# Performance work log

Hardware: AMD Instinct MI355X
Metric: run time of the kernel (lower is better)

## Reference

```python
import jax, jax.numpy as jnp
import numpy as np

# dims
B, S, D, H, DH, M, L, V, BS, NR = 4, 2048, 512, 8, 64, 2048, 6, 32000, 64, 3
NB = S // BS  # 32 blocks


def _block_plan(nb, seed):
    """BigBird block connectivity: 2 global + 3 window + NR random blocks per query block.
    Returns idx [nb, K] int32 and validity mask [nb, K] bool (dedup + edge handling)."""
    rng = np.random.RandomState(seed)
    K = 5 + NR
    idx = np.zeros((nb, K), np.int32)
    msk = np.zeros((nb, K), bool)
    for i in range(nb):
        fixed = {0, nb - 1} | {j for j in (i - 1, i, i + 1) if 0 <= j < nb}
        rest = [j for j in range(nb) if j not in fixed]
        rnd = rng.choice(rest, size=min(NR, len(rest)), replace=False) if rest else []
        sel = sorted(fixed | set(int(r) for r in rnd))
        idx[i, :len(sel)] = sel
        msk[i, :len(sel)] = True
    return jnp.asarray(idx), jnp.asarray(msk)


def _posemb():
    pos = np.arange(S, dtype=np.float32)[:, None]
    div = np.exp(np.arange(0, D, 2, dtype=np.float32) * (-np.log(10000.0) / D))
    pe = np.zeros((S, D), np.float32)
    pe[:, 0::2] = np.sin(pos * div)
    pe[:, 1::2] = np.cos(pos * div)
    return jnp.asarray(pe)


def _ln(x, scale, bias):
    m = jnp.mean(x, axis=-1, keepdims=True)
    v = jnp.mean(jnp.square(x - m), axis=-1, keepdims=True)
    return (x - m) * jax.lax.rsqrt(v + 1e-6) * scale + bias


def _bigbird_attn(x, key_mask, wq, wk, wv, wo, idx, bmask):
    # x: [B,S,D]; idx/bmask: [NB,K]
    q = jnp.einsum('bsd,dhe->bshe', x, wq).reshape(B, NB, BS, H, DH)
    k = jnp.einsum('bsd,dhe->bshe', x, wk).reshape(B, NB, BS, H, DH)
    v = jnp.einsum('bsd,dhe->bshe', x, wv).reshape(B, NB, BS, H, DH)
    kg = k[:, idx]  # [B,NB,K,BS,H,DH] gathered key blocks
    vg = v[:, idx]
    scores = jnp.einsum('bnqhe,bnkche->bhnqkc', q, kg) / jnp.sqrt(jnp.float32(DH))
    kmb = key_mask.reshape(B, NB, BS)[:, idx]          # [B,NB,K,BS]
    m = kmb & bmask[None, :, :, None]                   # [B,NB,K,BS]
    scores = jnp.where(m[:, None, :, None, :, :], scores, jnp.float32(-1e9))
    Kc = idx.shape[1]
    attn = jax.nn.softmax(scores.reshape(B, H, NB, BS, Kc * BS), axis=-1)
    attn = attn.reshape(B, H, NB, BS, Kc, BS)
    out = jnp.einsum('bhnqkc,bnkche->bnqhe', attn, vg).reshape(B, S, H, DH)
    return jnp.einsum('bshe,hed->bsd', out, wo)


def setup_inputs() -> dict:
    key = jax.random.key(0)
    ks = jax.random.split(key, 12)
    n = jax.random.normal
    inp = {
        'tokens': jax.random.randint(ks[0], (B, S), 0, V, dtype=jnp.int32),
        'embed': n(ks[1], (V, D), dtype=jnp.float32),
        'ln1_s': jnp.ones((L, D), jnp.float32), 'ln1_b': jnp.zeros((L, D), jnp.float32),
        'wq': n(ks[2], (L, D, H, DH), dtype=jnp.float32) * 0.02,
        'wk': n(ks[3], (L, D, H, DH), dtype=jnp.float32) * 0.02,
        'wv': n(ks[4], (L, D, H, DH), dtype=jnp.float32) * 0.02,
        'wo': n(ks[5], (L, H, DH, D), dtype=jnp.float32) * 0.02,
        'ln2_s': jnp.ones((L, D), jnp.float32), 'ln2_b': jnp.zeros((L, D), jnp.float32),
        'w1': n(ks[6], (L, D, M), dtype=jnp.float32) * 0.02, 'b1': jnp.zeros((L, M), jnp.float32),
        'w2': n(ks[7], (L, M, D), dtype=jnp.float32) * 0.02, 'b2': jnp.zeros((L, D), jnp.float32),
        'lnf_s': jnp.ones((D,), jnp.float32), 'lnf_b': jnp.zeros((D,), jnp.float32),
    }
    return inp


def reference(tokens, embed, ln1_s, ln1_b, wq, wk, wv, wo, ln2_s, ln2_b, w1, b1, w2, b2, lnf_s, lnf_b):
    key_mask = tokens > 0                      # src padding mask
    x = embed[tokens] + _posemb()[None]        # [B,S,D]
    plans = [_block_plan(NB, l) for l in range(L)]  # connectivity_seed = layer index
    for l in range(L):
        idx, bm = plans[l]
        h = _ln(x, ln1_s[l], ln1_b[l])
        x = x + _bigbird_attn(h, key_mask, wq[l], wk[l], wv[l], wo[l], idx, bm)
        y = _ln(x, ln2_s[l], ln2_b[l])
        y = jax.nn.gelu(jnp.einsum('bsd,dm->bsm', y, w1[l]) + b1[l])
        y = jnp.einsum('bsm,md->bsd', y, w2[l]) + b2[l]
        x = x + y
    return _ln(x, lnf_s, lnf_b)
```

## Files before the change

kernel.cpp:

```cpp
#include <hip/hip_runtime.h>

using u32 = unsigned int;
using u16 = unsigned short;

#define B_   4
#define S_   2048
#define D_   512
#define H_   8
#define DH_  64
#define FF_  2048
#define L_   6
#define NB_  32
#define KC_  8

typedef __attribute__((ext_vector_type(8))) __bf16 bf16x8;
typedef __attribute__((ext_vector_type(4))) float  f32x4;

struct Plan { unsigned char idx[NB_][KC_]; unsigned char cnt[NB_]; };

#define QSCALE 0.18033688011112042f

__device__ __forceinline__ u16 f2b(float f) {
  union { __bf16 b; u16 u; } x;
  x.b = (__bf16)f;
  return x.u;
}
__device__ __forceinline__ float b2f(u16 u) {
  union { u32 u; float f; } x;
  x.u = ((u32)u) << 16;
  return x.f;
}

__device__ __forceinline__ float gelu_f(float x) {
  float y2 = 1.5957691216f * x + 0.0713548163f * x * x * x;
  return x / (1.0f + __expf(-y2));
}

typedef const __attribute__((address_space(1))) u32* gas_t;
typedef __attribute__((address_space(3))) u32* las_t;
__device__ __forceinline__ void glds16(const u16* g, u16* l) {
  __builtin_amdgcn_global_load_lds((gas_t)g, (las_t)l, 16, 0, 0);
}

__global__ __launch_bounds__(256)
void transpose_all(const float* __restrict__ wq, const float* __restrict__ wk,
                   const float* __restrict__ wv, const float* __restrict__ wo,
                   const float* __restrict__ w1, const float* __restrict__ w2,
                   u16* __restrict__ wqkvT, u16* __restrict__ woT,
                   u16* __restrict__ w1T, u16* __restrict__ w2T) {
  __shared__ float tile[32][33];
  const int l = blockIdx.z;
  int idx = blockIdx.x;
  const float* src;
  u16* dst;
  int R, C, rowoff;
  size_t lstride;
  if (idx < 768) {
    int w = idx >> 8; idx &= 255;
    src = (w == 0) ? wq : (w == 1) ? wk : wv;
    dst = wqkvT; R = 512; C = 512; lstride = (size_t)1536 * 512; rowoff = w * 512;
  } else if (idx < 1024) {
    idx -= 768;  src = wo; dst = woT; R = 512;  C = 512;  lstride = (size_t)512 * 512;  rowoff = 0;
  } else if (idx < 2048) {
    idx -= 1024; src = w1; dst = w1T; R = 512;  C = 2048; lstride = (size_t)2048 * 512; rowoff = 0;
  } else {
    idx -= 2048; src = w2; dst = w2T; R = 2048; C = 512;  lstride = (size_t)512 * 2048; rowoff = 0;
  }
  const int ntx = C >> 5;
  const int c0 = (idx % ntx) * 32, r0 = (idx / ntx) * 32;
  src += (size_t)l * R * C;
  dst += (size_t)l * lstride;
  const int tx = threadIdx.x, ty = threadIdx.y;
#pragma unroll
  for (int i = 0; i < 4; i++)
    tile[ty + i * 8][tx] = src[(size_t)(r0 + ty + i * 8) * C + c0 + tx];
  __syncthreads();
#pragma unroll
  for (int i = 0; i < 4; i++)
    dst[(size_t)(rowoff + c0 + ty + i * 8) * R + r0 + tx] = f2b(tile[tx][ty + i * 8]);
}

__global__ __launch_bounds__(128)
void embed_ln(const int* __restrict__ tokens, const float* __restrict__ emb,
              const float* __restrict__ lns, const float* __restrict__ lnb,
              u16* __restrict__ x, u16* __restrict__ h) {
  const int row = blockIdx.x;
  const int s = row & (S_ - 1);
  const int t = threadIdx.x;
  const int tok = tokens[row];
  float4 v = ((const float4*)(emb + (size_t)tok * D_))[t];
  float va[4] = {v.x, v.y, v.z, v.w};
  const float cc = -2.0f * logf(10000.0f) / (float)D_;
  const float pos = (float)s;
#pragma unroll
  for (int j = 0; j < 4; j++) {
    int d = t * 4 + j;
    int i = d >> 1;
    float dv = expf(cc * (float)i);
    float ang = pos * dv;
    va[j] += (d & 1) ? cosf(ang) : sinf(ang);
  }
  ushort4 xb;
  xb.x = f2b(va[0]); xb.y = f2b(va[1]); xb.z = f2b(va[2]); xb.w = f2b(va[3]);
  ((ushort4*)x)[(size_t)row * (D_ / 4) + t] = xb;

  float sm = va[0] + va[1] + va[2] + va[3];
  float sq = va[0] * va[0] + va[1] * va[1] + va[2] * va[2] + va[3] * va[3];
#pragma unroll
  for (int d = 1; d < 64; d <<= 1) {
    sm += __shfl_xor(sm, d);
    sq += __shfl_xor(sq, d);
  }
  __shared__ float red[4];
  const int wv_ = t >> 6, lane = t & 63;
  if (lane == 0) { red[wv_ * 2] = sm; red[wv_ * 2 + 1] = sq; }
  __syncthreads();
  const float ts  = red[0] + red[2];
  const float tsq = red[1] + red[3];
  const float mean = ts * (1.0f / (float)D_);
  const float inv  = rsqrtf(tsq * (1.0f / (float)D_) - mean * mean + 1e-6f);
  const int d0 = t * 4;
  ushort4 u;
  u.x = f2b((va[0] - mean) * inv * lns[d0 + 0] + lnb[d0 + 0]);
  u.y = f2b((va[1] - mean) * inv * lns[d0 + 1] + lnb[d0 + 1]);
  u.z = f2b((va[2] - mean) * inv * lns[d0 + 2] + lnb[d0 + 2]);
  u.w = f2b((va[3] - mean) * inv * lns[d0 + 3] + lnb[d0 + 3]);
  ((ushort4*)h)[(size_t)row * (D_ / 4) + t] = u;
}

template <bool BF16OUT>
__global__ __launch_bounds__(128)
void ln_kernel(const u16* __restrict__ x, const float* __restrict__ sc,
               const float* __restrict__ bi, void* __restrict__ outp) {
  const int row = blockIdx.x;
  const int t = threadIdx.x;
  ushort4 xb = ((const ushort4*)(x + (size_t)row * D_))[t];
  float va[4] = {b2f(xb.x), b2f(xb.y), b2f(xb.z), b2f(xb.w)};
  float s = va[0] + va[1] + va[2] + va[3];
  float sq = va[0] * va[0] + va[1] * va[1] + va[2] * va[2] + va[3] * va[3];
#pragma unroll
  for (int d = 1; d < 64; d <<= 1) {
    s  += __shfl_xor(s, d);
    sq += __shfl_xor(sq, d);
  }
  __shared__ float red[4];
  const int wv = t >> 6, lane = t & 63;
  if (lane == 0) { red[wv * 2] = s; red[wv * 2 + 1] = sq; }
  __syncthreads();
  const float ts  = red[0] + red[2];
  const float tsq = red[1] + red[3];
  const float mean = ts * (1.0f / (float)D_);
  const float inv  = rsqrtf(tsq * (1.0f / (float)D_) - mean * mean + 1e-6f);
  const int d0 = t * 4;
  float o[4];
#pragma unroll
  for (int j = 0; j < 4; j++)
    o[j] = (va[j] - mean) * inv * sc[d0 + j] + bi[d0 + j];
  if (BF16OUT) {
    ushort4 u;
    u.x = f2b(o[0]); u.y = f2b(o[1]); u.z = f2b(o[2]); u.w = f2b(o[3]);
    ((ushort4*)outp)[(size_t)row * (D_ / 4) + t] = u;
  } else {
    ((float4*)outp)[(size_t)row * (D_ / 4) + t] = make_float4(o[0], o[1], o[2], o[3]);
  }
}

template <int MODE, bool VSPLIT, int TM, int TN>
__global__ __launch_bounds__(TN * 2)
void gemm_pipe(const u16* __restrict__ A, const u16* __restrict__ BT,
               int Kk, int ostride, int ncols,
               u16* __restrict__ outb,
               const float* __restrict__ bias, const u16* __restrict__ resid,
               u16* __restrict__ vtout) {
  constexpr int NW  = TN / 32;
  constexpr int WC  = NW / 2;
  constexpr int MI  = TM / 32;
  constexpr int CHA = TM / (8 * NW);
  constexpr int CHB = TN / (8 * NW);
  constexpr int VM  = CHA + CHB;
  __shared__ u16 As[2][TM * 64];
  __shared__ u16 Bs[2][TN * 64];
  const int tid = threadIdx.x;
  const int wave = tid >> 6, lane = tid & 63;
  const int nwg = gridDim.x, cpx = nwg >> 3;
  const int bid = blockIdx.x;
  const int gid = (bid & 7) * cpx + (bid >> 3);
  const int row0 = (gid / ncols) * TM, col0 = (gid % ncols) * TN;
  const int wr = wave / WC, wc = wave % WC;
  const int l15 = lane & 15, l4 = lane >> 4;

  const u16* asrc[CHA];
  const u16* bsrc[CHB];
  int adst[CHA], bdst[CHB];
#pragma unroll
  for (int i = 0; i < CHA; i++) {
    int chunk = wave * (CHA * 64) + i * 64 + lane;
    int r = chunk >> 3, s = chunk & 7;
    asrc[i] = A + (size_t)(row0 + r) * Kk + ((s ^ (r & 7)) << 3);
    adst[i] = (wave * (CHA * 64) + i * 64) * 8;
  }
#pragma unroll
  for (int i = 0; i < CHB; i++) {
    int chunk = wave * (CHB * 64) + i * 64 + lane;
    int r = chunk >> 3, s = chunk & 7;
    bsrc[i] = BT + (size_t)(col0 + r) * Kk + ((s ^ (r & 7)) << 3);
    bdst[i] = (wave * (CHB * 64) + i * 64) * 8;
  }

  int aoff[MI], boff[4];
#pragma unroll
  for (int m = 0; m < MI; m++) aoff[m] = (wr * (MI * 16) + m * 16 + l15) * 64;
#pragma unroll
  for (int n = 0; n < 4; n++) boff[n] = (wc * 64 + n * 16 + l15) * 64;
  const int sk0 = ((l4)     ^ (l15 & 7)) << 3;
  const int sk1 = ((4 + l4) ^ (l15 & 7)) << 3;

  f32x4 acc[MI][4] = {};
  const int nk = Kk >> 6;

  auto stage = [&](int buf, int kt) {
    const int ko = kt << 6;
#pragma unroll
    for (int i = 0; i < CHA; i++) glds16(asrc[i] + ko, &As[buf][adst[i]]);
#pragma unroll
    for (int i = 0; i < CHB; i++) glds16(bsrc[i] + ko, &Bs[buf][bdst[i]]);
  };

  stage(0, 0);
  stage(1, 1);

  for (int kt = 0; kt < nk; ++kt) {
    const int cur = kt & 1;
    if (kt + 1 < nk) {
      if constexpr (VM == 8) { asm volatile("s_waitcnt vmcnt(8)" ::: "memory"); }
      else                   { asm volatile("s_waitcnt vmcnt(6)" ::: "memory"); }
    } else {
      asm volatile("s_waitcnt vmcnt(0)" ::: "memory");
    }
    __builtin_amdgcn_s_barrier();
    __builtin_amdgcn_sched_barrier(0);

    bf16x8 af0[MI], bf0[4];
#pragma unroll
    for (int m = 0; m < MI; m++) af0[m] = *(const bf16x8*)&As[cur][aoff[m] + sk0];
#pragma unroll
    for (int n = 0; n < 4; n++) bf0[n] = *(const bf16x8*)&Bs[cur][boff[n] + sk0];
#pragma unroll
    for (int m = 0; m < MI; m++)
#pragma unroll
      for (int n = 0; n < 4; n++)
        acc[m][n] = __builtin_amdgcn_mfma_f32_16x16x32_bf16(af0[m], bf0[n], acc[m][n], 0, 0, 0);

    bf16x8 af1[MI], bf1[4];
#pragma unroll
    for (int m = 0; m < MI; m++) af1[m] = *(const bf16x8*)&As[cur][aoff[m] + sk1];
#pragma unroll
    for (int n = 0; n < 4; n++) bf1[n] = *(const bf16x8*)&Bs[cur][boff[n] + sk1];
    asm volatile("s_waitcnt lgkmcnt(0)" ::: "memory");
    __builtin_amdgcn_sched_barrier(0);
    __builtin_amdgcn_s_barrier();
    __builtin_amdgcn_sched_barrier(0);
    if (kt + 2 < nk) stage(cur, kt + 2);

    __builtin_amdgcn_s_setprio(1);
#pragma unroll
    for (int m = 0; m < MI; m++)
#pragma unroll
      for (int n = 0; n < 4; n++)
        acc[m][n] = __builtin_amdgcn_mfma_f32_16x16x32_bf16(af1[m], bf1[n], acc[m][n], 0, 0, 0);
    __builtin_amdgcn_s_setprio(0);
  }

#pragma unroll
  for (int m = 0; m < MI; m++) {
#pragma unroll
    for (int n = 0; n < 4; n++) {
      const int c = col0 + wc * 64 + n * 16 + l15;
      const int rb = row0 + wr * (MI * 16) + m * 16 + l4 * 4;
      if (VSPLIT && c >= 1024) {
        u16 pk[4];
#pragma unroll
        for (int j = 0; j < 4; j++) pk[j] = f2b(acc[m][n][j]);
        *(uint2*)(vtout + (size_t)(c - 1024) * (B_ * S_) + rb) = *(const uint2*)pk;
      } else {
#pragma unroll
        for (int j = 0; j < 4; j++) {
          const size_t o = (size_t)(rb + j) * ostride + c;
          float v = acc[m][n][j];
          if (MODE == 0) {
            if (VSPLIT && c < 512) v *= QSCALE;
            outb[o] = f2b(v);
          } else if (MODE == 1) {
            outb[o] = f2b(v + b2f(resid[o]));
          } else if (MODE == 2) {
            outb[o] = f2b(gelu_f(v + bias[c]));
          } else {
            outb[o] = f2b(v + bias[c] + b2f(resid[o]));
          }
        }
      }
    }
  }
}

__global__ __launch_bounds__(256, 4)
void attn_mfma(const u16* __restrict__ qkv, const u16* __restrict__ vTg,
               const int* __restrict__ tokens, u16* __restrict__ outb, Plan plan) {
  __shared__ u16 ks[2][64 * 64];
  __shared__ u16 vt[2][64 * 64];
  __shared__ u16 ps[64 * 64];

  const int blk = blockIdx.x;
  const int h0 = blk & 7;
  const int n  = (blk >> 3) & 31;
  const int b  = blk >> 8;
  const int t  = threadIdx.x;
  const int wave = t >> 6, lane = t & 63;
  const int l15 = lane & 15, l4 = lane >> 4;
  const int ncnt = plan.cnt[n];
  const int qrow0 = b * S_ + n * 64;

  auto stage = [&](int bi, int c, int* tkd) {
    const int krow0 = b * S_ + c * 64;
#pragma unroll
    for (int i = 0; i < 2; i++) {
      int c0 = i * 256 + wave * 64;
      int cl = c0 + lane;
      int r = cl >> 3, s = cl & 7;
      int sw = (s ^ (r & 7)) << 3;
      glds16(qkv + (size_t)(krow0 + r) * 1024 + 512 + h0 * 64 + sw, &ks[bi][c0 * 8]);
      glds16(vTg + (size_t)(h0 * 64 + r) * (B_ * S_) + krow0 + sw, &vt[bi][c0 * 8]);
    }
#pragma unroll
    for (int nn = 0; nn < 4; nn++) tkd[nn] = tokens[krow0 + nn * 16 + l15];
  };

  bf16x8 qaf[2];
#pragma unroll
  for (int ks_ = 0; ks_ < 2; ks_++)
    qaf[ks_] = *(const bf16x8*)(qkv + (size_t)(qrow0 + wave * 16 + l15) * 1024 +
                                h0 * 64 + ks_ * 32 + l4 * 8);

  int tk[4], tn[4];
  stage(0, plan.idx[n][0], tk);

  f32x4 oacc[4] = {};
  float mrow[4], lrow[4];
#pragma unroll
  for (int j = 0; j < 4; j++) { mrow[j] = -3e38f; lrow[j] = 0.0f; }

  for (int kc = 0; kc < ncnt; kc++) {
    const int cur = kc & 1;
    __syncthreads();
    if (kc + 1 < ncnt) stage(cur ^ 1, plan.idx[n][kc + 1], tn);

    f32x4 sacc[4] = {};
#pragma unroll
    for (int nn = 0; nn < 4; nn++) {
      int r = nn * 16 + l15;
#pragma unroll
      for (int ks_ = 0; ks_ < 2; ks_++) {
        bf16x8 kf = *(const bf16x8*)(&ks[cur][r * 64 + ((ks_ * 32 + l4 * 8) ^ ((r & 7) << 3))]);
        sacc[nn] = __builtin_amdgcn_mfma_f32_16x16x32_bf16(qaf[ks_], kf, sacc[nn], 0, 0, 0);
      }
    }

    bool vld[4];
#pragma unroll
    for (int nn = 0; nn < 4; nn++) vld[nn] = tk[nn] > 0;

    float rmax[4];
#pragma unroll
    for (int j = 0; j < 4; j++) {
      float mj = -3e38f;
#pragma unroll
      for (int nn = 0; nn < 4; nn++)
        if (vld[nn]) mj = fmaxf(mj, sacc[nn][j]);
      rmax[j] = mj;
    }
#pragma unroll
    for (int d = 1; d < 16; d <<= 1) {
#pragma unroll
      for (int j = 0; j < 4; j++) rmax[j] = fmaxf(rmax[j], __shfl_xor(rmax[j], d));
    }
    int chg = 0;
#pragma unroll
    for (int j = 0; j < 4; j++) chg |= (rmax[j] > mrow[j] + 8.0f);
    if (__ballot(chg)) {
#pragma unroll
      for (int j = 0; j < 4; j++) {
        float mn = fmaxf(mrow[j], rmax[j]);
        float alpha = exp2f(mrow[j] - mn);
        mrow[j] = mn;
        lrow[j] *= alpha;
#pragma unroll
        for (int n2 = 0; n2 < 4; n2++) oacc[n2][j] *= alpha;
      }
    }
    float p[4][4];
#pragma unroll
    for (int j = 0; j < 4; j++) {
      float psum = 0.0f;
#pragma unroll
      for (int nn = 0; nn < 4; nn++) {
        float pv = vld[nn] ? exp2f(sacc[nn][j] - mrow[j]) : 0.0f;
        p[nn][j] = pv;
        psum += pv;
      }
      lrow[j] += psum;
    }

#pragma unroll
    for (int nn = 0; nn < 4; nn++)
#pragma unroll
      for (int j = 0; j < 4; j++) {
        int q = wave * 16 + l4 * 4 + j;
        ps[q * 64 + ((nn * 16 + l15) ^ ((q & 7) << 3))] = f2b(p[nn][j]);
      }

#pragma unroll
    for (int ks_ = 0; ks_ < 2; ks_++) {
      int r = wave * 16 + l15;
      bf16x8 paf = *(const bf16x8*)(ps + r * 64 + ((ks_ * 32 + l4 * 8) ^ ((r & 7) << 3)));
#pragma unroll
      for (int n2 = 0; n2 < 4; n2++) {
        int rv = n2 * 16 + l15;
        bf16x8 vf = *(const bf16x8*)(&vt[cur][rv * 64 + ((ks_ * 32 + l4 * 8) ^ ((rv & 7) << 3))]);
        oacc[n2] = __builtin_amdgcn_mfma_f32_16x16x32_bf16(paf, vf, oacc[n2], 0, 0, 0);
      }
    }
#pragma unroll
    for (int nn = 0; nn < 4; nn++) tk[nn] = tn[nn];
  }

#pragma unroll
  for (int d = 1; d < 16; d <<= 1) {
#pragma unroll
    for (int j = 0; j < 4; j++) lrow[j] += __shfl_xor(lrow[j], d);
  }
#pragma unroll
  for (int j = 0; j < 4; j++) {
    const float inv = lrow[j] > 0.0f ? 1.0f / lrow[j] : 0.0f;
    const int q = n * 64 + wave * 16 + l4 * 4 + j;
#pragma unroll
    for (int n2 = 0; n2 < 4; n2++) {
      outb[(size_t)(b * S_ + q) * D_ + h0 * 64 + n2 * 16 + l15] = f2b(oacc[n2][j] * inv);
    }
  }
}

namespace {
struct HostMT {
  u32 mt[624]; int mti;
  void seed(u32 s) {
    mt[0] = s;
    for (int i = 1; i < 624; i++)
      mt[i] = 1812433253u * (mt[i - 1] ^ (mt[i - 1] >> 30)) + (u32)i;
    mti = 624;
  }
  u32 next() {
    if (mti >= 624) {
      for (int k = 0; k < 624; k++) {
        u32 y = (mt[k] & 0x80000000u) | (mt[(k + 1) % 624] & 0x7fffffffu);
        mt[k] = mt[(k + 397) % 624] ^ (y >> 1) ^ ((y & 1u) ? 0x9908b0dfu : 0u);
      }
      mti = 0;
    }
    u32 y = mt[mti++];
    y ^= y >> 11;
    y ^= (y << 7)  & 0x9d2c5680u;
    y ^= (y << 15) & 0xefc60000u;
    y ^= y >> 18;
    return y;
  }
  u32 interval(u32 mx) {
    if (mx == 0u) return 0u;
    u32 mask = mx;
    mask |= mask >> 1; mask |= mask >> 2; mask |= mask >> 4;
    mask |= mask >> 8; mask |= mask >> 16;
    u32 v;
    while ((v = (next() & mask)) > mx) {}
    return v;
  }
};

void build_plan(int l, Plan* out) {
  HostMT rng;
  rng.seed((u32)l);
  for (int i = 0; i < NB_; i++) {
    bool fixedv[NB_] = {};
    fixedv[0] = true; fixedv[NB_ - 1] = true;
    for (int j = i - 1; j <= i + 1; j++)
      if (j >= 0 && j < NB_) fixedv[j] = true;
    int rest[NB_]; int nr = 0;
    for (int j = 0; j < NB_; j++) if (!fixedv[j]) rest[nr++] = j;
    int perm[NB_];
    for (int tt = 0; tt < nr; tt++) perm[tt] = tt;
    for (int tt = nr - 1; tt >= 1; tt--) {
      int j = (int)rng.interval((u32)tt);
      int tmp = perm[tt]; perm[tt] = perm[j]; perm[j] = tmp;
    }
    bool sel[NB_];
    for (int j = 0; j < NB_; j++) sel[j] = fixedv[j];
    for (int c = 0; c < 3; c++) sel[rest[perm[c]]] = true;
    int cnt = 0;
    for (int j = 0; j < NB_; j++)
      if (sel[j]) out->idx[i][cnt++] = (unsigned char)j;
    out->cnt[i] = (unsigned char)cnt;
    for (int c2 = cnt; c2 < KC_; c2++) out->idx[i][c2] = 0;
  }
}
}

extern "C" void kernel_launch(void* const* d_in, const int* in_sizes, int n_in,
                              void* d_out, int out_size, void* d_ws, size_t ws_size,
                              hipStream_t stream) {
  (void)in_sizes; (void)n_in; (void)out_size; (void)ws_size;

  const int*   tokens = (const int*)d_in[0];
  const float* embed  = (const float*)d_in[1];
  const float* ln1_s  = (const float*)d_in[2];
  const float* ln1_b  = (const float*)d_in[3];
  const float* wq     = (const float*)d_in[4];
  const float* wk     = (const float*)d_in[5];
  const float* wv     = (const float*)d_in[6];
  const float* wo     = (const float*)d_in[7];
  const float* ln2_s  = (const float*)d_in[8];
  const float* ln2_b  = (const float*)d_in[9];
  const float* w1     = (const float*)d_in[10];
  const float* b1     = (const float*)d_in[11];
  const float* w2     = (const float*)d_in[12];
  const float* b2     = (const float*)d_in[13];
  const float* lnf_s  = (const float*)d_in[14];
  const float* lnf_b  = (const float*)d_in[15];

  char* wp = (char*)d_ws;
  auto take = [&](size_t bytes) {
    void* p = (void*)wp;
    wp += (bytes + 255) & ~(size_t)255;
    return p;
  };

  const int Mrows = B_ * S_;
  u16* wqkvT = (u16*)take((size_t)L_ * 1536 * D_ * 2);
  u16* woT   = (u16*)take((size_t)L_ * D_ * D_ * 2);
  u16* w1T   = (u16*)take((size_t)L_ * FF_ * D_ * 2);
  u16* w2T   = (u16*)take((size_t)L_ * D_ * FF_ * 2);
  u16* x     = (u16*)take((size_t)Mrows * D_ * 2);
  u16* h     = (u16*)take((size_t)Mrows * D_ * 2);
  u16* big   = (u16*)take((size_t)Mrows * FF_ * 2);
  u16* qkv   = big;
  u16* vT    = big + (size_t)Mrows * 1024;
  u16* g     = big;

  Plan plans[L_];
  for (int l = 0; l < L_; l++) build_plan(l, &plans[l]);

  const size_t qkvL = (size_t)1536 * D_;

  transpose_all<<<dim3(3072, 1, L_), dim3(32, 8), 0, stream>>>(
      wq, wk, wv, wo, w1, w2, wqkvT, woT, w1T, w2T);
  embed_ln<<<Mrows, 128, 0, stream>>>(tokens, embed, ln1_s, ln1_b, x, h);

  for (int l = 0; l < L_; l++) {
    gemm_pipe<0, true, 128, 128><<<768, 256, 0, stream>>>(
        h, wqkvT + (size_t)l * qkvL, D_, 1024, 12, qkv, nullptr, nullptr, vT);
    attn_mfma<<<B_ * NB_ * H_, 256, 0, stream>>>(qkv, vT, tokens, h, plans[l]);
    gemm_pipe<1, false, 64, 128><<<512, 256, 0, stream>>>(
        h, woT + (size_t)l * D_ * D_, D_, D_, 4, x, nullptr, x, nullptr);
    ln_kernel<true><<<Mrows, 128, 0, stream>>>(x, ln2_s + l * D_, ln2_b + l * D_, h);
    gemm_pipe<2, false, 128, 128><<<1024, 256, 0, stream>>>(
        h, w1T + (size_t)l * FF_ * D_, D_, FF_, 16, g, b1 + l * FF_, nullptr, nullptr);
    gemm_pipe<3, false, 64, 128><<<512, 256, 0, stream>>>(
        g, w2T + (size_t)l * D_ * FF_, FF_, D_, 4, x, b2 + l * D_, x, nullptr);
    if (l + 1 < L_)
      ln_kernel<true><<<Mrows, 128, 0, stream>>>(x, ln1_s + (l + 1) * D_, ln1_b + (l + 1) * D_, h);
  }
  ln_kernel<false><<<Mrows, 128, 0, stream>>>(x, lnf_s, lnf_b, d_out);
}
```

Before: 840.4 us.

## Fold LayerNorm into GEMMs via weight scaling and epilogue row statistics

Removes the standalone LayerNorm kernels. The LN scale is folded into the transposed QKV and W1 weights, and per-column bias terms (beta·W and column sums) are precomputed. The following GEMM epilogue then applies mean and rstd correction to the raw residual input. The residual-producing GEMMs emit partial per-row sum and sum-of-squares into a stats buffer, saving one read and write pass of the activations per LN. In exchange it adds a one-time uv precompute kernel and epilogue overhead, and it risks precision loss from the E[x²]−mean² variance form and from feeding unnormalized bf16 x into the GEMM.

```diff
diff --git a/kernel.cpp b/kernel.cpp
--- a/kernel.cpp
+++ b/kernel.cpp
@@ -46,6 +46,7 @@
 void transpose_all(const float* __restrict__ wq, const float* __restrict__ wk,
                    const float* __restrict__ wv, const float* __restrict__ wo,
                    const float* __restrict__ w1, const float* __restrict__ w2,
+                   const float* __restrict__ ln1_s, const float* __restrict__ ln2_s,
                    u16* __restrict__ wqkvT, u16* __restrict__ woT,
                    u16* __restrict__ w1T, u16* __restrict__ w2T) {
   __shared__ float tile[32][33];
@@ -55,14 +56,17 @@
   u16* dst;
   int R, C, rowoff;
   size_t lstride;
+  const float* gam = nullptr;
   if (idx < 768) {
     int w = idx >> 8; idx &= 255;
     src = (w == 0) ? wq : (w == 1) ? wk : wv;
     dst = wqkvT; R = 512; C = 512; lstride = (size_t)1536 * 512; rowoff = w * 512;
+    gam = ln1_s + l * 512;
   } else if (idx < 1024) {
     idx -= 768;  src = wo; dst = woT; R = 512;  C = 512;  lstride = (size_t)512 * 512;  rowoff = 0;
   } else if (idx < 2048) {
     idx -= 1024; src = w1; dst = w1T; R = 512;  C = 2048; lstride = (size_t)2048 * 512; rowoff = 0;
+    gam = ln2_s + l * 512;
   } else {
     idx -= 2048; src = w2; dst = w2T; R = 2048; C = 512;  lstride = (size_t)512 * 2048; rowoff = 0;
   }
@@ -75,15 +79,57 @@
   for (int i = 0; i < 4; i++)
     tile[ty + i * 8][tx] = src[(size_t)(r0 + ty + i * 8) * C + c0 + tx];
   __syncthreads();
+  const float gsc = gam ? gam[r0 + tx] : 1.0f;
 #pragma unroll
   for (int i = 0; i < 4; i++)
-    dst[(size_t)(rowoff + c0 + ty + i * 8) * R + r0 + tx] = f2b(tile[tx][ty + i * 8]);
+    dst[(size_t)(rowoff + c0 + ty + i * 8) * R + r0 + tx] = f2b(tile[tx][ty + i * 8] * gsc);
+}
+
+__global__ __launch_bounds__(64)
+void compute_uv(const float* __restrict__ wq, const float* __restrict__ wk,
+                const float* __restrict__ wv, const float* __restrict__ w1,
+                const float* __restrict__ ln1_b, const float* __restrict__ ln2_b,
+                const u16* __restrict__ wqkvT, const u16* __restrict__ w1T,
+                float* __restrict__ uvq, float* __restrict__ uv1) {
+  const int gid = blockIdx.x;
+  const int l = gid / 3584, n = gid % 3584;
+  const int t = threadIdx.x;
+  const float* W; const float* beta; const u16* WT; float* uv; int C;
+  if (n < 1536) {
+    int w = n >> 9, nc = n & 511;
+    W = ((w == 0) ? wq : (w == 1) ? wk : wv) + (size_t)l * 512 * 512 + nc;
+    C = 512;
+    beta = ln1_b + l * 512;
+    WT = wqkvT + ((size_t)l * 1536 + n) * 512;
+    uv = uvq + ((size_t)l * 1536 + n) * 2;
+  } else {
+    int nc = n - 1536;
+    W = w1 + (size_t)l * 512 * 2048 + nc;
+    C = 2048;
+    beta = ln2_b + l * 512;
+    WT = w1T + ((size_t)l * 2048 + nc) * 512;
+    uv = uv1 + ((size_t)l * 2048 + nc) * 2;
+  }
+  float uu = 0.0f, vv = 0.0f;
+  for (int k = t; k < 512; k += 64)
+    uu = fmaf(beta[k], W[(size_t)k * C], uu);
+  const uint4* wt4 = (const uint4*)WT;
+  {
+    uint4 u4 = wt4[t];
+    u32 us[4] = {u4.x, u4.y, u4.z, u4.w};
+#pragma unroll
+    for (int z = 0; z < 4; z++) {
+      vv += b2f((u16)(us[z] & 0xffffu)) + b2f((u16)(us[z] >> 16));
+    }
+  }
+#pragma unroll
+  for (int d = 1; d < 64; d <<= 1) { uu += __shfl_xor(uu, d); vv += __shfl_xor(vv, d); }
+  if (t == 0) { uv[0] = uu; uv[1] = vv; }
 }
 
 __global__ __launch_bounds__(128)
-void embed_ln(const int* __restrict__ tokens, const float* __restrict__ emb,
-              const float* __restrict__ lns, const float* __restrict__ lnb,
-              u16* __restrict__ x, u16* __restrict__ h) {
+void embed_stats(const int* __restrict__ tokens, const float* __restrict__ emb,
+                 u16* __restrict__ x, float* __restrict__ pstats) {
   const int row = blockIdx.x;
   const int s = row & (S_ - 1);
   const int t = threadIdx.x;
@@ -115,63 +161,45 @@
   const int wv_ = t >> 6, lane = t & 63;
   if (lane == 0) { red[wv_ * 2] = sm; red[wv_ * 2 + 1] = sq; }
   __syncthreads();
-  const float ts  = red[0] + red[2];
-  const float tsq = red[1] + red[3];
-  const float mean = ts * (1.0f / (float)D_);
-  const float inv  = rsqrtf(tsq * (1.0f / (float)D_) - mean * mean + 1e-6f);
-  const int d0 = t * 4;
-  ushort4 u;
-  u.x = f2b((va[0] - mean) * inv * lns[d0 + 0] + lnb[d0 + 0]);
-  u.y = f2b((va[1] - mean) * inv * lns[d0 + 1] + lnb[d0 + 1]);
-  u.z = f2b((va[2] - mean) * inv * lns[d0 + 2] + lnb[d0 + 2]);
-  u.w = f2b((va[3] - mean) * inv * lns[d0 + 3] + lnb[d0 + 3]);
-  ((ushort4*)h)[(size_t)row * (D_ / 4) + t] = u;
-}
-
-template <bool BF16OUT>
+  if (t < 8) {
+    pstats[(size_t)row * 16 + t * 2]     = (t == 0) ? (red[0] + red[2]) : 0.0f;
+    pstats[(size_t)row * 16 + t * 2 + 1] = (t == 0) ? (red[1] + red[3]) : 0.0f;
+  }
+}
+
 __global__ __launch_bounds__(128)
-void ln_kernel(const u16* __restrict__ x, const float* __restrict__ sc,
-               const float* __restrict__ bi, void* __restrict__ outp) {
+void ln_final(const u16* __restrict__ x, const float* __restrict__ pstats,
+              const float* __restrict__ sc, const float* __restrict__ bi,
+              float* __restrict__ outp) {
   const int row = blockIdx.x;
   const int t = threadIdx.x;
+  float s = 0.0f, q = 0.0f;
+#pragma unroll
+  for (int i = 0; i < 8; i++) {
+    s += pstats[(size_t)row * 16 + i * 2];
+    q += pstats[(size_t)row * 16 + i * 2 + 1];
+  }
+  const float mean = s * (1.0f / (float)D_);
+  const float inv  = rsqrtf(q * (1.0f / (float)D_) - mean * mean + 1e-6f);
   ushort4 xb = ((const ushort4*)(x + (size_t)row * D_))[t];
   float va[4] = {b2f(xb.x), b2f(xb.y), b2f(xb.z), b2f(xb.w)};
-  float s = va[0] + va[1] + va[2] + va[3];
-  float sq = va[0] * va[0] + va[1] * va[1] + va[2] * va[2] + va[3] * va[3];
-#pragma unroll
-  for (int d = 1; d < 64; d <<= 1) {
-    s  += __shfl_xor(s, d);
-    sq += __shfl_xor(sq, d);
-  }
-  __shared__ float red[4];
-  const int wv = t >> 6, lane = t & 63;
-  if (lane == 0) { red[wv * 2] = s; red[wv * 2 + 1] = sq; }
-  __syncthreads();
-  const float ts  = red[0] + red[2];
-  const float tsq = red[1] + red[3];
-  const float mean = ts * (1.0f / (float)D_);
-  const float inv  = rsqrtf(tsq * (1.0f / (float)D_) - mean * mean + 1e-6f);
   const int d0 = t * 4;
   float o[4];
 #pragma unroll
   for (int j = 0; j < 4; j++)
     o[j] = (va[j] - mean) * inv * sc[d0 + j] + bi[d0 + j];
-  if (BF16OUT) {
-    ushort4 u;
-    u.x = f2b(o[0]); u.y = f2b(o[1]); u.z = f2b(o[2]); u.w = f2b(o[3]);
-    ((ushort4*)outp)[(size_t)row * (D_ / 4) + t] = u;
-  } else {
-    ((float4*)outp)[(size_t)row * (D_ / 4) + t] = make_float4(o[0], o[1], o[2], o[3]);
-  }
-}
-
-template <int MODE, bool VSPLIT, int TM, int TN>
+  ((float4*)outp)[(size_t)row * (D_ / 4) + t] = make_float4(o[0], o[1], o[2], o[3]);
+}
+
+template <int MODE, bool VSPLIT, int TM, int TN, bool FOLD, bool STATS>
 __global__ __launch_bounds__(TN * 2)
 void gemm_pipe(const u16* __restrict__ A, const u16* __restrict__ BT,
                int Kk, int ostride, int ncols,
                u16* __restrict__ outb,
                const float* __restrict__ bias, const u16* __restrict__ resid,
-               u16* __restrict__ vtout) {
+               u16* __restrict__ vtout,
+               const float* __restrict__ uv, const float* __restrict__ pstats_in,
+               float* __restrict__ pstats_out) {
   constexpr int NW  = TN / 32;
   constexpr int WC  = NW / 2;
   constexpr int MI  = TM / 32;
@@ -271,35 +299,95 @@
     __builtin_amdgcn_s_setprio(0);
   }
 
+  float* sl = nullptr;
+  float* mi = nullptr;
+  if constexpr (FOLD) {
+    __syncthreads();
+    sl = (float*)&As[0][0];
+    mi = sl + TM * 16;
+    for (int i = tid; i < TM * 16; i += TN * 2)
+      sl[i] = pstats_in[(size_t)row0 * 16 + i];
+    __syncthreads();
+    if (tid < TM) {
+      float s = 0.0f, q = 0.0f;
+#pragma unroll
+      for (int t2 = 0; t2 < 8; t2++) { s += sl[tid * 16 + t2 * 2]; q += sl[tid * 16 + t2 * 2 + 1]; }
+      const float mu = s * (1.0f / (float)D_);
+      mi[tid * 2] = mu;
+      mi[tid * 2 + 1] = rsqrtf(q * (1.0f / (float)D_) - mu * mu + 1e-6f);
+    }
+    __syncthreads();
+  }
+
+  float rs[MI][4], rq[MI][4];
+  if constexpr (STATS) {
+#pragma unroll
+    for (int m = 0; m < MI; m++)
+#pragma unroll
+      for (int j = 0; j < 4; j++) { rs[m][j] = 0.0f; rq[m][j] = 0.0f; }
+  }
+
 #pragma unroll
   for (int m = 0; m < MI; m++) {
 #pragma unroll
     for (int n = 0; n < 4; n++) {
       const int c = col0 + wc * 64 + n * 16 + l15;
       const int rb = row0 + wr * (MI * 16) + m * 16 + l4 * 4;
+      float vals[4];
+#pragma unroll
+      for (int j = 0; j < 4; j++) {
+        float v = acc[m][n][j];
+        if constexpr (FOLD) {
+          const int rl = wr * (MI * 16) + m * 16 + l4 * 4 + j;
+          const float mu = mi[rl * 2], iv = mi[rl * 2 + 1];
+          const float2 uvc = ((const float2*)uv)[c];
+          v = v * iv + uvc.x - mu * iv * uvc.y;
+        }
+        vals[j] = v;
+      }
       if (VSPLIT && c >= 1024) {
         u16 pk[4];
 #pragma unroll
-        for (int j = 0; j < 4; j++) pk[j] = f2b(acc[m][n][j]);
+        for (int j = 0; j < 4; j++) pk[j] = f2b(vals[j]);
         *(uint2*)(vtout + (size_t)(c - 1024) * (B_ * S_) + rb) = *(const uint2*)pk;
       } else {
 #pragma unroll
         for (int j = 0; j < 4; j++) {
           const size_t o = (size_t)(rb + j) * ostride + c;
-          float v = acc[m][n][j];
+          float v = vals[j];
           if (MODE == 0) {
             if (VSPLIT && c < 512) v *= QSCALE;
             outb[o] = f2b(v);
           } else if (MODE == 1) {
-            outb[o] = f2b(v + b2f(resid[o]));
+            v = v + b2f(resid[o]);
+            outb[o] = f2b(v);
           } else if (MODE == 2) {
             outb[o] = f2b(gelu_f(v + bias[c]));
           } else {
-            outb[o] = f2b(v + bias[c] + b2f(resid[o]));
+            v = v + bias[c] + b2f(resid[o]);
+            outb[o] = f2b(v);
           }
+          if constexpr (STATS) { rs[m][j] += v; rq[m][j] += v * v; }
         }
       }
     }
+  }
+
+  if constexpr (STATS) {
+#pragma unroll
+    for (int m = 0; m < MI; m++)
+#pragma unroll
+      for (int j = 0; j < 4; j++) {
+        float s = rs[m][j], q = rq[m][j];
+#pragma unroll
+        for (int d = 1; d < 16; d <<= 1) { s += __shfl_xor(s, d); q += __shfl_xor(q, d); }
+        if (l15 == 0) {
+          const int r = row0 + wr * (MI * 16) + m * 16 + l4 * 4 + j;
+          const int slot = (col0 + wc * 64) >> 6;
+          pstats_out[(size_t)r * 16 + slot * 2]     = s;
+          pstats_out[(size_t)r * 16 + slot * 2 + 1] = q;
+        }
+      }
   }
 }
 
@@ -548,6 +636,9 @@
   u16* w2T   = (u16*)take((size_t)L_ * D_ * FF_ * 2);
   u16* x     = (u16*)take((size_t)Mrows * D_ * 2);
   u16* h     = (u16*)take((size_t)Mrows * D_ * 2);
+  float* pstats = (float*)take((size_t)Mrows * 16 * 4);
+  float* uvq = (float*)take((size_t)L_ * 1536 * 2 * 4);
+  float* uv1 = (float*)take((size_t)L_ * 2048 * 2 * 4);
   u16* big   = (u16*)take((size_t)Mrows * FF_ * 2);
   u16* qkv   = big;
   u16* vT    = big + (size_t)Mrows * 1024;
@@ -559,22 +650,25 @@
   const size_t qkvL = (size_t)1536 * D_;
 
   transpose_all<<<dim3(3072, 1, L_), dim3(32, 8), 0, stream>>>(
-      wq, wk, wv, wo, w1, w2, wqkvT, woT, w1T, w2T);
-  embed_ln<<<Mrows, 128, 0, stream>>>(tokens, embed, ln1_s, ln1_b, x, h);
+      wq, wk, wv, wo, w1, w2, ln1_s, ln2_s, wqkvT, woT, w1T, w2T);
+  compute_uv<<<L_ * 3584, 64, 0, stream>>>(
+      wq, wk, wv, w1, ln1_b, ln2_b, wqkvT, w1T, uvq, uv1);
+  embed_stats<<<Mrows, 128, 0, stream>>>(tokens, embed, x, pstats);
 
   for (int l = 0; l < L_; l++) {
-    gemm_pipe<0, true, 128, 128><<<768, 256, 0, stream>>>(
-        h, wqkvT + (size_t)l * qkvL, D_, 1024, 12, qkv, nullptr, nullptr, vT);
+    gemm_pipe<0, true, 128, 128, true, false><<<768, 256, 0, stream>>>(
+        x, wqkvT + (size_t)l * qkvL, D_, 1024, 12, qkv, nullptr, nullptr, vT,
+        uvq + (size_t)l * 1536 * 2, pstats, nullptr);
     attn_mfma<<<B_ * NB_ * H_, 256, 0, stream>>>(qkv, vT, tokens, h, plans[l]);
-    gemm_pipe<1, false, 64, 128><<<512, 256, 0, stream>>>(
-        h, woT + (size_t)l * D_ * D_, D_, D_, 4, x, nullptr, x, nullptr);
-    ln_kernel<true><<<Mrows, 128, 0, stream>>>(x, ln2_s + l * D_, ln2_b + l * D_, h);
-    gemm_pipe<2, false, 128, 128><<<1024, 256, 0, stream>>>(
-        h, w1T + (size_t)l * FF_ * D_, D_, FF_, 16, g, b1 + l * FF_, nullptr, nullptr);
-    gemm_pipe<3, false, 64, 128><<<512, 256, 0, stream>>>(
-        g, w2T + (size_t)l * D_ * FF_, FF_, D_, 4, x, b2 + l * D_, x, nullptr);
-    if (l + 1 < L_)
-      ln_kernel<true><<<Mrows, 128, 0, stream>>>(x, ln1_s + (l + 1) * D_, ln1_b + (l + 1) * D_, h);
-  }
-  ln_kernel<false><<<Mrows, 128, 0, stream>>>(x, lnf_s, lnf_b, d_out);
-}
+    gemm_pipe<1, false, 64, 128, false, true><<<512, 256, 0, stream>>>(
+        h, woT + (size_t)l * D_ * D_, D_, D_, 4, x, nullptr, x, nullptr,
+        nullptr, nullptr, pstats);
+    gemm_pipe<2, false, 128, 128, true, false><<<1024, 256, 0, stream>>>(
+        x, w1T + (size_t)l * FF_ * D_, D_, FF_, 16, g, b1 + l * FF_, nullptr, nullptr,
+        uv1 + (size_t)l * 2048 * 2, pstats, nullptr);
+    gemm_pipe<3, false, 64, 128, false, true><<<512, 256, 0, stream>>>(
+        g, w2T + (size_t)l * D_ * FF_, FF_, D_, 4, x, b2 + l * D_, x, nullptr,
+        nullptr, nullptr, pstats);
+  }
+  ln_final<<<Mrows, 128, 0, stream>>>(x, pstats, lnf_s, lnf_b, (float*)d_out);
+}
```

After: 874.3 us. +4.0%, slower.
